# Kernel optimization log

Measured on AMD Instinct MI355X. Metric: run time of the kernel, lower is better.

The kernel has to match this reference:

```python
import jax, jax.numpy as jnp
import numpy as np

D = 256          # num_channels
H = 4            # num_heads
DH = D // H      # head dim
BN_EPS = 1e-5


def conv1x1(x, W, b):
    # x: [B, Cin, N], W: [Cout, Cin], b: [Cout] -> [B, Cout, N]
    return jnp.einsum('oc,bcn->bon', W, x) + b[None, :, None]


def bn_eval(x, gamma, beta):
    # eval-mode BatchNorm1d with running_mean=0, running_var=1
    scale = gamma / jnp.sqrt(1.0 + BN_EPS)
    return x * scale[None, :, None] + beta[None, :, None]


def setup_inputs() -> dict:
    key = jax.random.key(0)
    ks = jax.random.split(key, 16)
    B, N = 1, 4096
    s = 0.05
    inp = {
        'corr_feat_belief': jax.random.normal(ks[0], (B, D, N), dtype=jnp.float32),
        'spatial_compatibility': jax.random.uniform(ks[1], (B, N, N), dtype=jnp.float32),
        'Wq': jax.random.normal(ks[2], (D, D), dtype=jnp.float32) * s,
        'bq': jnp.zeros((D,), jnp.float32),
        'Wk': jax.random.normal(ks[3], (D, D), dtype=jnp.float32) * s,
        'bk': jnp.zeros((D,), jnp.float32),
        'Wv': jax.random.normal(ks[4], (D, D), dtype=jnp.float32) * s,
        'bv': jnp.zeros((D,), jnp.float32),
        'W1': jax.random.normal(ks[5], (D // 2, D), dtype=jnp.float32) * s,
        'b1': jnp.zeros((D // 2,), jnp.float32),
        'g1': jnp.ones((D // 2,), jnp.float32),
        'be1': jnp.zeros((D // 2,), jnp.float32),
        'W2': jax.random.normal(ks[6], (D // 2, D // 2), dtype=jnp.float32) * s,
        'b2': jnp.zeros((D // 2,), jnp.float32),
        'g2': jnp.ones((D // 2,), jnp.float32),
        'be2': jnp.zeros((D // 2,), jnp.float32),
        'W3': jax.random.normal(ks[7], (D, D // 2), dtype=jnp.float32) * s,
        'b3': jnp.zeros((D,), jnp.float32),
    }
    return inp


def reference(corr_feat_belief, spatial_compatibility, Wq, bq, Wk, bk, Wv, bv,
              W1, b1, g1, be1, W2, b2, g2, be2, W3, b3):
    x = corr_feat_belief                      # [B, D, N]
    B, _, N = x.shape
    # QKV conv1x1 projections, split heads -> [B, H, DH, N]
    Q = conv1x1(x, Wq, bq).reshape(B, H, DH, N)
    K = conv1x1(x, Wk, bk).reshape(B, H, DH, N)
    V = conv1x1(x, Wv, bv).reshape(B, H, DH, N)
    # attention scores [B, H, N, N], scaled
    att = jnp.einsum('bhco,bhci->bhoi', Q, K) / np.sqrt(DH).astype(np.float32)
    # multiplicative spatial-compatibility mask, softmax over keys
    weight = jax.nn.softmax(spatial_compatibility[:, None, :, :] * att, axis=-1)
    message = jnp.einsum('bhoi,bhci->bhco', weight, V).reshape(B, D, N)
    # message MLP: conv1x1 -> BN -> ReLU -> conv1x1 -> BN -> ReLU -> conv1x1
    h = jax.nn.relu(bn_eval(conv1x1(message, W1, b1), g1, be1))
    h = jax.nn.relu(bn_eval(conv1x1(h, W2, b2), g2, be2))
    h = conv1x1(h, W3, b3)
    return x + h
```

## Files before the change

### kernel.cpp

```cpp
#include <hip/hip_runtime.h>
#include <hip/hip_bf16.h>
#include <math.h>

#define D_CH   256
#define NHEAD  4
#define DHEAD  64
#define NPTS   4096
#define KSPLIT 8
#define KCHUNK (NPTS / KSPLIT)
#define BN_RSQ 0.99999500003749963f
#define HSTRIDE 262144

typedef __attribute__((ext_vector_type(4))) float f32x4;
typedef __attribute__((ext_vector_type(8))) short bf16x8;
typedef unsigned short ushort_t;

__device__ __forceinline__ ushort_t f2bf(float x) {
    unsigned int b = __float_as_uint(x);
    return (ushort_t)((b + 0x7FFF + ((b >> 16) & 1)) >> 16);
}
__device__ __forceinline__ float bf2f(ushort_t u) {
    return __uint_as_float(((unsigned int)u) << 16);
}
__device__ __forceinline__ unsigned cvt_pk(float lo, float hi) {
    unsigned r;
    asm("v_cvt_pk_bf16_f32 %0, %1, %2" : "=v"(r) : "v"(lo), "v"(hi));
    return r;
}

__global__ __launch_bounds__(256) void transpose_cast(
    const float* __restrict__ x, ushort_t* __restrict__ xT)
{
    __shared__ float xs[64][65];
    const int tid = threadIdx.x;
    const int n0 = blockIdx.x * 64, k0 = blockIdx.y * 64;
#pragma unroll
    for (int p = 0; p < 16; ++p) {
        int kk = p * 4 + (tid >> 6), nn = tid & 63;
        xs[kk][nn] = x[(size_t)(k0 + kk) * NPTS + n0 + nn];
    }
    __syncthreads();
#pragma unroll
    for (int p = 0; p < 16; ++p) {
        int nn = p * 4 + (tid >> 6), kk = tid & 63;
        xT[(size_t)(n0 + nn) * D_CH + k0 + kk] = f2bf(xs[kk][nn]);
    }
}

__device__ __forceinline__ void gemm_tile_body(
    const float* __restrict__ A, const ushort_t* __restrict__ Bt,
    int K, int m0, int n0, int l15, int lhi, f32x4 acc[2][2])
{
#pragma unroll
    for (int i = 0; i < 2; ++i)
#pragma unroll
        for (int j = 0; j < 2; ++j) acc[i][j] = (f32x4){0.f, 0.f, 0.f, 0.f};

    for (int k0 = 0; k0 < K; k0 += 32) {
        bf16x8 af[2], bfr[2];
#pragma unroll
        for (int mf = 0; mf < 2; ++mf) {
            const float* ap = A + (size_t)(m0 + mf * 16 + l15) * K + k0 + lhi * 8;
            float4 a0 = *(const float4*)ap;
            float4 a1 = *(const float4*)(ap + 4);
            unsigned* tp = (unsigned*)&af[mf];
            tp[0] = cvt_pk(a0.x, a0.y);
            tp[1] = cvt_pk(a0.z, a0.w);
            tp[2] = cvt_pk(a1.x, a1.y);
            tp[3] = cvt_pk(a1.z, a1.w);
        }
#pragma unroll
        for (int nf = 0; nf < 2; ++nf)
            bfr[nf] = *(const bf16x8*)&Bt[(size_t)(n0 + nf * 16 + l15) * K + k0 + lhi * 8];
#pragma unroll
        for (int mf = 0; mf < 2; ++mf)
#pragma unroll
            for (int nf = 0; nf < 2; ++nf)
                acc[mf][nf] = __builtin_amdgcn_mfma_f32_16x16x32_bf16(af[mf], bfr[nf], acc[mf][nf], 0, 0, 0);
    }
}

__global__ __launch_bounds__(256) void gemm_qkv(
    const float* __restrict__ Wq, const float* __restrict__ bq,
    const float* __restrict__ Wk, const float* __restrict__ bk,
    const float* __restrict__ Wv, const float* __restrict__ bv,
    const ushort_t* __restrict__ xT,
    ushort_t* __restrict__ Qf, ushort_t* __restrict__ Kf, ushort_t* __restrict__ Vf)
{
    const int tid = threadIdx.x;
    const int w = tid >> 6, lane = tid & 63, l15 = lane & 15, lhi = lane >> 4;
    const int wm = w >> 1, wn = w & 1;
    const int m0 = blockIdx.y * 64 + wm * 32;
    const int n0 = blockIdx.x * 64 + wn * 32;
    const int z = blockIdx.z;

    const float* A    = (z == 0) ? Wq : (z == 1) ? Wk : Wv;
    const float* bias = (z == 0) ? bq : (z == 1) ? bk : bv;
    ushort_t* dst     = (z == 0) ? Qf : (z == 1) ? Kf : Vf;
    const float scl   = (z == 0) ? 0.125f : 1.0f;

    f32x4 acc[2][2];
    gemm_tile_body(A, xT, D_CH, m0, n0, l15, lhi, acc);

#pragma unroll
    for (int mf = 0; mf < 2; ++mf) {
#pragma unroll
        for (int r = 0; r < 4; ++r) {
            int m = m0 + mf * 16 + lhi * 4 + r;
            int head = m >> 6, dch = m & 63;
            float bi = bias[m];
#pragma unroll
            for (int nf = 0; nf < 2; ++nf) {
                int n = n0 + nf * 16 + l15;
                float v = (acc[mf][nf][r] + bi) * scl;
                size_t idx;
                if (z < 2)
                    idx = (size_t)head * HSTRIDE + (size_t)(n >> 4) * 1024 + (dch >> 5) * 512
                        + (((dch >> 3) & 3) * 16 + (n & 15)) * 8 + (dch & 7);
                else
                    idx = (size_t)head * HSTRIDE + (size_t)(n >> 6) * 4096 + (dch >> 4) * 1024
                        + ((n >> 5) & 1) * 512 + (((n >> 3) & 3) * 16 + (dch & 15)) * 8 + (n & 7);
                dst[idx] = (ushort_t)(cvt_pk(v, v) & 0xFFFF);
            }
        }
    }
}

__device__ __forceinline__ void attn_tile(
    int kt, int ktn, const float* __restrict__ Sg,
    const ushort_t* __restrict__ Kh, const ushort_t* __restrict__ Vh,
    const bf16x8 (&qf)[2][2],
    ushort_t (* __restrict__ Sw)[72],
    f32x4 (&macc)[2][4], float (&lrun)[2],
    ushort_t (* __restrict__ Pw)[72], int l15, int lhi, int lane)
{
    f32x4 sr[8];
#pragma unroll
    for (int p = 0; p < 8; ++p)
        sr[p] = *(const f32x4*)&Sg[(size_t)p * 4 * NPTS + (size_t)ktn * 64];

    f32x4 sacc0[4], sacc1[4];
    __builtin_amdgcn_s_setprio(1);
#pragma unroll
    for (int kb = 0; kb < 4; ++kb) {
        const ushort_t* kp = Kh + (size_t)(kt * 4 + kb) * 1024 + lane * 8;
        bf16x8 kf0 = *(const bf16x8*)kp;
        bf16x8 kf1 = *(const bf16x8*)(kp + 512);
        f32x4 z0 = (f32x4){0.f, 0.f, 0.f, 0.f};
        z0 = __builtin_amdgcn_mfma_f32_16x16x32_bf16(kf0, qf[0][0], z0, 0, 0, 0);
        z0 = __builtin_amdgcn_mfma_f32_16x16x32_bf16(kf1, qf[0][1], z0, 0, 0, 0);
        sacc0[kb] = z0;
        f32x4 z1 = (f32x4){0.f, 0.f, 0.f, 0.f};
        z1 = __builtin_amdgcn_mfma_f32_16x16x32_bf16(kf0, qf[1][0], z1, 0, 0, 0);
        z1 = __builtin_amdgcn_mfma_f32_16x16x32_bf16(kf1, qf[1][1], z1, 0, 0, 0);
        sacc1[kb] = z1;
    }
    __builtin_amdgcn_s_setprio(0);

    bf16x8 vf[8];
    const ushort_t* vb = Vh + (size_t)kt * 4096 + lane * 8;
#pragma unroll
    for (int mm = 0; mm < 2; ++mm)
#pragma unroll
        for (int db = 0; db < 4; ++db)
            vf[mm * 4 + db] = *(const bf16x8*)(vb + db * 1024 + mm * 512);

    float ts0 = 0.0f, ts1 = 0.0f;
#pragma unroll
    for (int kb = 0; kb < 4; ++kb) {
        unsigned a0 = *(const unsigned*)&Sw[l15][kb * 16 + lhi * 4];
        unsigned a1 = *(const unsigned*)&Sw[l15][kb * 16 + lhi * 4 + 2];
        unsigned b0 = *(const unsigned*)&Sw[16 + l15][kb * 16 + lhi * 4];
        unsigned b1 = *(const unsigned*)&Sw[16 + l15][kb * 16 + lhi * 4 + 2];
        float p00 = __expf(sacc0[kb][0] * bf2f((ushort_t)(a0 & 0xFFFF)));
        float p01 = __expf(sacc0[kb][1] * bf2f((ushort_t)(a0 >> 16)));
        float p02 = __expf(sacc0[kb][2] * bf2f((ushort_t)(a1 & 0xFFFF)));
        float p03 = __expf(sacc0[kb][3] * bf2f((ushort_t)(a1 >> 16)));
        float p10 = __expf(sacc1[kb][0] * bf2f((ushort_t)(b0 & 0xFFFF)));
        float p11 = __expf(sacc1[kb][1] * bf2f((ushort_t)(b0 >> 16)));
        float p12 = __expf(sacc1[kb][2] * bf2f((ushort_t)(b1 & 0xFFFF)));
        float p13 = __expf(sacc1[kb][3] * bf2f((ushort_t)(b1 >> 16)));
        ts0 += (p00 + p01) + (p02 + p03);
        ts1 += (p10 + p11) + (p12 + p13);
        *(unsigned*)&Pw[l15][kb * 16 + lhi * 4]          = cvt_pk(p00, p01);
        *(unsigned*)&Pw[l15][kb * 16 + lhi * 4 + 2]      = cvt_pk(p02, p03);
        *(unsigned*)&Pw[16 + l15][kb * 16 + lhi * 4]     = cvt_pk(p10, p11);
        *(unsigned*)&Pw[16 + l15][kb * 16 + lhi * 4 + 2] = cvt_pk(p12, p13);
    }
    lrun[0] += ts0;
    lrun[1] += ts1;

#pragma unroll
    for (int p = 0; p < 8; ++p) {
        *(unsigned*)&Sw[p * 4 + lhi][l15 * 4]     = cvt_pk(sr[p][0], sr[p][1]);
        *(unsigned*)&Sw[p * 4 + lhi][l15 * 4 + 2] = cvt_pk(sr[p][2], sr[p][3]);
    }

    __builtin_amdgcn_s_setprio(1);
#pragma unroll
    for (int mm = 0; mm < 2; ++mm) {
        bf16x8 pf0 = *(const bf16x8*)&Pw[l15][mm * 32 + lhi * 8];
        bf16x8 pf1 = *(const bf16x8*)&Pw[16 + l15][mm * 32 + lhi * 8];
#pragma unroll
        for (int db = 0; db < 4; ++db) {
            macc[0][db] = __builtin_amdgcn_mfma_f32_16x16x32_bf16(vf[mm * 4 + db], pf0, macc[0][db], 0, 0, 0);
            macc[1][db] = __builtin_amdgcn_mfma_f32_16x16x32_bf16(vf[mm * 4 + db], pf1, macc[1][db], 0, 0, 0);
        }
    }
    __builtin_amdgcn_s_setprio(0);
}

__global__ __launch_bounds__(256, 3) void attn_mfma(
    const ushort_t* __restrict__ Qf, const ushort_t* __restrict__ Kf,
    const ushort_t* __restrict__ Vf, const float* __restrict__ S,
    ushort_t* __restrict__ pacc, float* __restrict__ pl)
{
    __shared__ __align__(16) ushort_t P_lds[4][32][72];
    __shared__ __align__(16) ushort_t S_lds[4][32][72];

    const int tid  = threadIdx.x;
    const int w    = tid >> 6;
    const int lane = tid & 63;
    const int l15  = lane & 15;
    const int lhi  = lane >> 4;
    const int h    = blockIdx.y;
    const int ks   = blockIdx.z;
    const int q0   = blockIdx.x * 128 + w * 32;
    const int ktb  = ks * (KCHUNK / 64);

    const ushort_t* Kh = Kf + (size_t)h * HSTRIDE;
    const ushort_t* Vh = Vf + (size_t)h * HSTRIDE;
    const float* Sg = S + (size_t)(q0 + lhi) * NPTS + l15 * 4;
    ushort_t (* __restrict__ Pw)[72] = P_lds[w];
    ushort_t (* __restrict__ Sw)[72] = S_lds[w];

    bf16x8 qf[2][2];
#pragma unroll
    for (int f = 0; f < 2; ++f) {
        const ushort_t* qp = Qf + (size_t)h * HSTRIDE
                           + (size_t)((q0 + f * 16) >> 4) * 1024 + lane * 8;
        qf[f][0] = *(const bf16x8*)qp;
        qf[f][1] = *(const bf16x8*)(qp + 512);
    }

    f32x4 macc[2][4];
#pragma unroll
    for (int f = 0; f < 2; ++f)
#pragma unroll
        for (int db = 0; db < 4; ++db) macc[f][db] = (f32x4){0.f, 0.f, 0.f, 0.f};
    float lrun[2] = {0.0f, 0.0f};

    {
#pragma unroll
        for (int p = 0; p < 8; ++p) {
            f32x4 t = *(const f32x4*)&Sg[(size_t)p * 4 * NPTS + (size_t)ktb * 64];
            *(unsigned*)&Sw[p * 4 + lhi][l15 * 4]     = cvt_pk(t[0], t[1]);
            *(unsigned*)&Sw[p * 4 + lhi][l15 * 4 + 2] = cvt_pk(t[2], t[3]);
        }
    }

    for (int kt = ktb; kt < ktb + 8; ++kt) {
        const int ktn = (kt + 1 < ktb + 8) ? kt + 1 : ktb;
        attn_tile(kt, ktn, Sg, Kh, Vh, qf, Sw, macc, lrun, Pw, l15, lhi, lane);
    }

#pragma unroll
    for (int f = 0; f < 2; ++f) {
        lrun[f] += __shfl_xor(lrun[f], 16);
        lrun[f] += __shfl_xor(lrun[f], 32);
    }

    const size_t pb = ((size_t)ks * NHEAD + h) * NPTS;
#pragma unroll
    for (int f = 0; f < 2; ++f) {
        ushort_t* prow = pacc + (pb + q0 + f * 16 + l15) * DHEAD;
#pragma unroll
        for (int db = 0; db < 4; ++db) {
            *(unsigned*)&prow[db * 16 + lhi * 4]     = cvt_pk(macc[f][db][0], macc[f][db][1]);
            *(unsigned*)&prow[db * 16 + lhi * 4 + 2] = cvt_pk(macc[f][db][2], macc[f][db][3]);
        }
    }
    if (lane < 16) {
        pl[pb + q0 + lane]      = lrun[0];
        pl[pb + q0 + 16 + lane] = lrun[1];
    }
}

__global__ __launch_bounds__(256) void mlp_fused(
    const ushort_t* __restrict__ pacc, const float* __restrict__ pl,
    ushort_t* __restrict__ msgT,
    const float* __restrict__ W1, const float* __restrict__ b1,
    const float* __restrict__ g1, const float* __restrict__ be1,
    const float* __restrict__ W2, const float* __restrict__ b2,
    const float* __restrict__ g2, const float* __restrict__ be2,
    const float* __restrict__ W3, const float* __restrict__ b3,
    const float* __restrict__ x, float* __restrict__ out,
    ushort_t* __restrict__ h1T, ushort_t* __restrict__ h2T)
{
    const int tid = threadIdx.x;
    const int w = tid >> 6, lane = tid & 63, l15 = lane & 15, lhi = lane >> 4;
    const int nblk = blockIdx.x * 32;

    {
        const int ql = tid >> 3;
        const int d0 = (tid & 7) * 8;
#pragma unroll
        for (int h = 0; h < NHEAD; ++h) {
            float ls = 0.0f;
#pragma unroll
            for (int ks = 0; ks < KSPLIT; ++ks)
                ls += pl[((size_t)ks * NHEAD + h) * NPTS + nblk + ql];
            float inv = 1.0f / ls;
            float o[8];
#pragma unroll
            for (int j = 0; j < 8; ++j) o[j] = 0.0f;
#pragma unroll
            for (int ks = 0; ks < KSPLIT; ++ks) {
                const ushort_t* ap = pacc
                    + (((size_t)ks * NHEAD + h) * NPTS + nblk + ql) * DHEAD + d0;
                bf16x8 v = *(const bf16x8*)ap;
#pragma unroll
                for (int j = 0; j < 8; ++j) o[j] += bf2f((ushort_t)v[j]);
            }
            unsigned* dp = (unsigned*)(msgT + (size_t)(nblk + ql) * D_CH + h * 64 + d0);
            dp[0] = cvt_pk(o[0] * inv, o[1] * inv);
            dp[1] = cvt_pk(o[2] * inv, o[3] * inv);
            dp[2] = cvt_pk(o[4] * inv, o[5] * inv);
            dp[3] = cvt_pk(o[6] * inv, o[7] * inv);
        }
    }
    __syncthreads();

    {
        f32x4 acc[2][2];
        gemm_tile_body(W1, msgT + (size_t)nblk * D_CH, D_CH, w * 32, 0, l15, lhi, acc);
#pragma unroll
        for (int mf = 0; mf < 2; ++mf)
#pragma unroll
            for (int r = 0; r < 4; ++r) {
                int m = w * 32 + mf * 16 + lhi * 4 + r;
                float bi = b1[m], sc = g1[m] * BN_RSQ, sh = be1[m];
#pragma unroll
                for (int nf = 0; nf < 2; ++nf) {
                    int n = nf * 16 + l15;
                    float v = fmaxf((acc[mf][nf][r] + bi) * sc + sh, 0.0f);
                    h1T[(size_t)(nblk + n) * 128 + m] = (ushort_t)(cvt_pk(v, v) & 0xFFFF);
                }
            }
    }
    __syncthreads();

    {
        f32x4 acc[2][2];
        gemm_tile_body(W2, h1T + (size_t)nblk * 128, 128, w * 32, 0, l15, lhi, acc);
#pragma unroll
        for (int mf = 0; mf < 2; ++mf)
#pragma unroll
            for (int r = 0; r < 4; ++r) {
                int m = w * 32 + mf * 16 + lhi * 4 + r;
                float bi = b2[m], sc = g2[m] * BN_RSQ, sh = be2[m];
#pragma unroll
                for (int nf = 0; nf < 2; ++nf) {
                    int n = nf * 16 + l15;
                    float v = fmaxf((acc[mf][nf][r] + bi) * sc + sh, 0.0f);
                    h2T[(size_t)(nblk + n) * 128 + m] = (ushort_t)(cvt_pk(v, v) & 0xFFFF);
                }
            }
    }
    __syncthreads();

#pragma unroll
    for (int half = 0; half < 2; ++half) {
        f32x4 acc[2][2];
        const int m0 = w * 64 + half * 32;
        gemm_tile_body(W3, h2T + (size_t)nblk * 128, 128, m0, 0, l15, lhi, acc);
#pragma unroll
        for (int mf = 0; mf < 2; ++mf)
#pragma unroll
            for (int r = 0; r < 4; ++r) {
                int m = m0 + mf * 16 + lhi * 4 + r;
                float bi = b3[m];
#pragma unroll
                for (int nf = 0; nf < 2; ++nf) {
                    int n = nblk + nf * 16 + l15;
                    out[(size_t)m * NPTS + n] = acc[mf][nf][r] + bi + x[(size_t)m * NPTS + n];
                }
            }
    }
}

extern "C" void kernel_launch(void* const* d_in, const int* in_sizes, int n_in,
                              void* d_out, int out_size, void* d_ws, size_t ws_size,
                              hipStream_t stream) {
    const float* x  = (const float*)d_in[0];
    const float* S  = (const float*)d_in[1];
    const float* Wq = (const float*)d_in[2];
    const float* bq = (const float*)d_in[3];
    const float* Wk = (const float*)d_in[4];
    const float* bk = (const float*)d_in[5];
    const float* Wv = (const float*)d_in[6];
    const float* bv = (const float*)d_in[7];
    const float* W1 = (const float*)d_in[8];
    const float* b1 = (const float*)d_in[9];
    const float* g1 = (const float*)d_in[10];
    const float* be1= (const float*)d_in[11];
    const float* W2 = (const float*)d_in[12];
    const float* b2 = (const float*)d_in[13];
    const float* g2 = (const float*)d_in[14];
    const float* be2= (const float*)d_in[15];
    const float* W3 = (const float*)d_in[16];
    const float* b3 = (const float*)d_in[17];

    char* ws = (char*)d_ws;
    const size_t MB = 1024 * 1024;
    ushort_t* xT   = (ushort_t*)(ws);
    ushort_t* Qf   = (ushort_t*)(ws + 2 * MB);
    ushort_t* Kf   = (ushort_t*)(ws + 4 * MB);
    ushort_t* Vf   = (ushort_t*)(ws + 6 * MB);
    ushort_t* pacc = (ushort_t*)(ws + 8 * MB);
    float*    pl   = (float*)   (ws + 24 * MB);
    ushort_t* msgT = (ushort_t*)(ws + 25 * MB);
    ushort_t* h1T  = (ushort_t*)(ws + 27 * MB);
    ushort_t* h2T  = (ushort_t*)(ws + 28 * MB);

    transpose_cast<<<dim3(64, 4), 256, 0, stream>>>(x, xT);
    gemm_qkv<<<dim3(64, 4, 3), 256, 0, stream>>>(Wq, bq, Wk, bk, Wv, bv, xT, Qf, Kf, Vf);

    attn_mfma<<<dim3(32, NHEAD, KSPLIT), 256, 0, stream>>>(Qf, Kf, Vf, S, pacc, pl);

    mlp_fused<<<dim3(128), 256, 0, stream>>>(pacc, pl, msgT,
        W1, b1, g1, be1, W2, b2, g2, be2, W3, b3, x, (float*)d_out, h1T, h2T);
}
```

Measured before the change: 97.99 us.

## Halve MLP point tile to double grid and reorder attention tile loads

```diff
diff --git a/kernel.cpp b/kernel.cpp
--- a/kernel.cpp
+++ b/kernel.cpp
@@ -138,6 +138,14 @@
 #pragma unroll
     for (int p = 0; p < 8; ++p)
         sr[p] = *(const f32x4*)&Sg[(size_t)p * 4 * NPTS + (size_t)ktn * 64];
+
+    bf16x8 vf[8];
+    const ushort_t* vb = Vh + (size_t)kt * 4096 + lane * 8;
+#pragma unroll
+    for (int mm = 0; mm < 2; ++mm)
+#pragma unroll
+        for (int db = 0; db < 4; ++db)
+            vf[mm * 4 + db] = *(const bf16x8*)(vb + db * 1024 + mm * 512);
 
     f32x4 sacc0[4], sacc1[4];
     __builtin_amdgcn_s_setprio(1);
@@ -156,14 +164,6 @@
         sacc1[kb] = z1;
     }
     __builtin_amdgcn_s_setprio(0);
-
-    bf16x8 vf[8];
-    const ushort_t* vb = Vh + (size_t)kt * 4096 + lane * 8;
-#pragma unroll
-    for (int mm = 0; mm < 2; ++mm)
-#pragma unroll
-        for (int db = 0; db < 4; ++db)
-            vf[mm * 4 + db] = *(const bf16x8*)(vb + db * 1024 + mm * 512);
 
     float ts0 = 0.0f, ts1 = 0.0f;
 #pragma unroll
@@ -190,24 +190,24 @@
     lrun[0] += ts0;
     lrun[1] += ts1;
 
+    __builtin_amdgcn_s_setprio(1);
+#pragma unroll
+    for (int mm = 0; mm < 2; ++mm) {
+        bf16x8 pf0 = *(const bf16x8*)&Pw[l15][mm * 32 + lhi * 8];
+        bf16x8 pf1 = *(const bf16x8*)&Pw[16 + l15][mm * 32 + lhi * 8];
+#pragma unroll
+        for (int db = 0; db < 4; ++db) {
+            macc[0][db] = __builtin_amdgcn_mfma_f32_16x16x32_bf16(vf[mm * 4 + db], pf0, macc[0][db], 0, 0, 0);
+            macc[1][db] = __builtin_amdgcn_mfma_f32_16x16x32_bf16(vf[mm * 4 + db], pf1, macc[1][db], 0, 0, 0);
+        }
+    }
+    __builtin_amdgcn_s_setprio(0);
+
 #pragma unroll
     for (int p = 0; p < 8; ++p) {
         *(unsigned*)&Sw[p * 4 + lhi][l15 * 4]     = cvt_pk(sr[p][0], sr[p][1]);
         *(unsigned*)&Sw[p * 4 + lhi][l15 * 4 + 2] = cvt_pk(sr[p][2], sr[p][3]);
     }
-
-    __builtin_amdgcn_s_setprio(1);
-#pragma unroll
-    for (int mm = 0; mm < 2; ++mm) {
-        bf16x8 pf0 = *(const bf16x8*)&Pw[l15][mm * 32 + lhi * 8];
-        bf16x8 pf1 = *(const bf16x8*)&Pw[16 + l15][mm * 32 + lhi * 8];
-#pragma unroll
-        for (int db = 0; db < 4; ++db) {
-            macc[0][db] = __builtin_amdgcn_mfma_f32_16x16x32_bf16(vf[mm * 4 + db], pf0, macc[0][db], 0, 0, 0);
-            macc[1][db] = __builtin_amdgcn_mfma_f32_16x16x32_bf16(vf[mm * 4 + db], pf1, macc[1][db], 0, 0, 0);
-        }
-    }
-    __builtin_amdgcn_s_setprio(0);
 }
 
 __global__ __launch_bounds__(256, 3) void attn_mfma(
@@ -299,13 +299,16 @@
 {
     const int tid = threadIdx.x;
     const int w = tid >> 6, lane = tid & 63, l15 = lane & 15, lhi = lane >> 4;
-    const int nblk = blockIdx.x * 32;
+    const int nblk = blockIdx.x * 16;
 
     {
-        const int ql = tid >> 3;
-        const int d0 = (tid & 7) * 8;
-#pragma unroll
-        for (int h = 0; h < NHEAD; ++h) {
+        const int hb  = (tid >> 7) * 2;
+        const int loc = tid & 127;
+        const int ql  = loc >> 3;
+        const int d0  = (loc & 7) * 8;
+#pragma unroll
+        for (int hh = 0; hh < 2; ++hh) {
+            const int h = hb + hh;
             float ls = 0.0f;
 #pragma unroll
             for (int ks = 0; ks < KSPLIT; ++ks)
@@ -332,59 +335,94 @@
     __syncthreads();
 
     {
-        f32x4 acc[2][2];
-        gemm_tile_body(W1, msgT + (size_t)nblk * D_CH, D_CH, w * 32, 0, l15, lhi, acc);
+        f32x4 acc[2];
+        acc[0] = (f32x4){0.f, 0.f, 0.f, 0.f};
+        acc[1] = (f32x4){0.f, 0.f, 0.f, 0.f};
+        const ushort_t* Bt = msgT + (size_t)nblk * D_CH;
+        for (int k0 = 0; k0 < 256; k0 += 32) {
+            bf16x8 bfr = *(const bf16x8*)&Bt[(size_t)l15 * D_CH + k0 + lhi * 8];
+#pragma unroll
+            for (int mf = 0; mf < 2; ++mf) {
+                const float* ap = W1 + (size_t)(w * 32 + mf * 16 + l15) * 256 + k0 + lhi * 8;
+                float4 a0 = *(const float4*)ap;
+                float4 a1 = *(const float4*)(ap + 4);
+                bf16x8 af;
+                unsigned* tp = (unsigned*)&af;
+                tp[0] = cvt_pk(a0.x, a0.y); tp[1] = cvt_pk(a0.z, a0.w);
+                tp[2] = cvt_pk(a1.x, a1.y); tp[3] = cvt_pk(a1.z, a1.w);
+                acc[mf] = __builtin_amdgcn_mfma_f32_16x16x32_bf16(af, bfr, acc[mf], 0, 0, 0);
+            }
+        }
 #pragma unroll
         for (int mf = 0; mf < 2; ++mf)
 #pragma unroll
             for (int r = 0; r < 4; ++r) {
                 int m = w * 32 + mf * 16 + lhi * 4 + r;
                 float bi = b1[m], sc = g1[m] * BN_RSQ, sh = be1[m];
-#pragma unroll
-                for (int nf = 0; nf < 2; ++nf) {
-                    int n = nf * 16 + l15;
-                    float v = fmaxf((acc[mf][nf][r] + bi) * sc + sh, 0.0f);
-                    h1T[(size_t)(nblk + n) * 128 + m] = (ushort_t)(cvt_pk(v, v) & 0xFFFF);
-                }
+                float v = fmaxf((acc[mf][r] + bi) * sc + sh, 0.0f);
+                h1T[(size_t)(nblk + l15) * 128 + m] = (ushort_t)(cvt_pk(v, v) & 0xFFFF);
             }
     }
     __syncthreads();
 
     {
-        f32x4 acc[2][2];
-        gemm_tile_body(W2, h1T + (size_t)nblk * 128, 128, w * 32, 0, l15, lhi, acc);
+        f32x4 acc[2];
+        acc[0] = (f32x4){0.f, 0.f, 0.f, 0.f};
+        acc[1] = (f32x4){0.f, 0.f, 0.f, 0.f};
+        const ushort_t* Bt = h1T + (size_t)nblk * 128;
+        for (int k0 = 0; k0 < 128; k0 += 32) {
+            bf16x8 bfr = *(const bf16x8*)&Bt[(size_t)l15 * 128 + k0 + lhi * 8];
+#pragma unroll
+            for (int mf = 0; mf < 2; ++mf) {
+                const float* ap = W2 + (size_t)(w * 32 + mf * 16 + l15) * 128 + k0 + lhi * 8;
+                float4 a0 = *(const float4*)ap;
+                float4 a1 = *(const float4*)(ap + 4);
+                bf16x8 af;
+                unsigned* tp = (unsigned*)&af;
+                tp[0] = cvt_pk(a0.x, a0.y); tp[1] = cvt_pk(a0.z, a0.w);
+                tp[2] = cvt_pk(a1.x, a1.y); tp[3] = cvt_pk(a1.z, a1.w);
+                acc[mf] = __builtin_amdgcn_mfma_f32_16x16x32_bf16(af, bfr, acc[mf], 0, 0, 0);
+            }
+        }
 #pragma unroll
         for (int mf = 0; mf < 2; ++mf)
 #pragma unroll
             for (int r = 0; r < 4; ++r) {
                 int m = w * 32 + mf * 16 + lhi * 4 + r;
                 float bi = b2[m], sc = g2[m] * BN_RSQ, sh = be2[m];
-#pragma unroll
-                for (int nf = 0; nf < 2; ++nf) {
-                    int n = nf * 16 + l15;
-                    float v = fmaxf((acc[mf][nf][r] + bi) * sc + sh, 0.0f);
-                    h2T[(size_t)(nblk + n) * 128 + m] = (ushort_t)(cvt_pk(v, v) & 0xFFFF);
-                }
+                float v = fmaxf((acc[mf][r] + bi) * sc + sh, 0.0f);
+                h2T[(size_t)(nblk + l15) * 128 + m] = (ushort_t)(cvt_pk(v, v) & 0xFFFF);
             }
     }
     __syncthreads();
 
-#pragma unroll
-    for (int half = 0; half < 2; ++half) {
-        f32x4 acc[2][2];
-        const int m0 = w * 64 + half * 32;
-        gemm_tile_body(W3, h2T + (size_t)nblk * 128, 128, m0, 0, l15, lhi, acc);
-#pragma unroll
-        for (int mf = 0; mf < 2; ++mf)
+    {
+        f32x4 acc[4];
+#pragma unroll
+        for (int i = 0; i < 4; ++i) acc[i] = (f32x4){0.f, 0.f, 0.f, 0.f};
+        const ushort_t* Bt = h2T + (size_t)nblk * 128;
+        for (int k0 = 0; k0 < 128; k0 += 32) {
+            bf16x8 bfr = *(const bf16x8*)&Bt[(size_t)l15 * 128 + k0 + lhi * 8];
+#pragma unroll
+            for (int mf = 0; mf < 4; ++mf) {
+                const float* ap = W3 + (size_t)(w * 64 + mf * 16 + l15) * 128 + k0 + lhi * 8;
+                float4 a0 = *(const float4*)ap;
+                float4 a1 = *(const float4*)(ap + 4);
+                bf16x8 af;
+                unsigned* tp = (unsigned*)&af;
+                tp[0] = cvt_pk(a0.x, a0.y); tp[1] = cvt_pk(a0.z, a0.w);
+                tp[2] = cvt_pk(a1.x, a1.y); tp[3] = cvt_pk(a1.z, a1.w);
+                acc[mf] = __builtin_amdgcn_mfma_f32_16x16x32_bf16(af, bfr, acc[mf], 0, 0, 0);
+            }
+        }
+#pragma unroll
+        for (int mf = 0; mf < 4; ++mf)
 #pragma unroll
             for (int r = 0; r < 4; ++r) {
-                int m = m0 + mf * 16 + lhi * 4 + r;
+                int m = w * 64 + mf * 16 + lhi * 4 + r;
                 float bi = b3[m];
-#pragma unroll
-                for (int nf = 0; nf < 2; ++nf) {
-                    int n = nblk + nf * 16 + l15;
-                    out[(size_t)m * NPTS + n] = acc[mf][nf][r] + bi + x[(size_t)m * NPTS + n];
-                }
+                int n = nblk + l15;
+                out[(size_t)m * NPTS + n] = acc[mf][r] + bi + x[(size_t)m * NPTS + n];
             }
     }
 }
@@ -428,6 +466,6 @@
 
     attn_mfma<<<dim3(32, NHEAD, KSPLIT), 256, 0, stream>>>(Qf, Kf, Vf, S, pacc, pl);
 
-    mlp_fused<<<dim3(128), 256, 0, stream>>>(pacc, pl, msgT,
+    mlp_fused<<<dim3(256), 256, 0, stream>>>(pacc, pl, msgT,
         W1, b1, g1, be1, W2, b2, g2, be2, W3, b3, x, (float*)d_out, h1T, h2T);
 }
```

Result: no change. 97.79 us (-0.2%).
